# Performance work log

Measured on AMD Instinct MI355X. Metric: run time of the kernel, lower is better.

The kernel has to match this reference:

```python
import jax, jax.numpy as jnp
import numpy as np

N_NODES = 100000
N_HEDGES = 10000
D = 128  # i_d = v_d = e_d = q_d
NUM_CLASS = 10
E = 640000


def _linear_params(key, d_in, d_out):
    k1, k2 = jax.random.split(key)
    lim = 1.0 / np.sqrt(d_in)
    W = jax.random.uniform(k1, (d_in, d_out), jnp.float32, -lim, lim)
    b = jax.random.uniform(k2, (d_out,), jnp.float32, -lim, lim)
    return W, b


def setup_inputs() -> dict:
    key = jax.random.key(0)
    ks = jax.random.split(key, 12)
    vfeat = jax.random.normal(ks[0], (N_NODES, D), jnp.float32)
    efeat = jax.random.normal(ks[1], (N_HEDGES, D), jnp.float32)
    he_idx = jax.random.randint(ks[2], (E,), 0, N_HEDGES, jnp.int32)
    nd_idx = jax.random.randint(ks[3], (E,), 0, N_NODES, jnp.int32)
    Wfl, bfl = _linear_params(ks[4], D, D)   # first_layer_in: i_d -> v_d
    W1, b1 = _linear_params(ks[5], D, D)     # w1: e_d -> q_d
    W2, b2 = _linear_params(ks[6], D, D)     # w2: v_d -> q_d
    W3, b3 = _linear_params(ks[7], D, D)     # w3: v_d -> e_d
    W4, b4 = _linear_params(ks[8], D, D)     # w4: v_d -> q_d
    W5, b5 = _linear_params(ks[9], D, D)     # w5: e_d -> q_d
    W6, b6 = _linear_params(ks[10], D, D)    # w6: e_d -> v_d
    Wc, bc = _linear_params(ks[11], D, NUM_CLASS)
    return dict(vfeat=vfeat, efeat=efeat, he_idx=he_idx, nd_idx=nd_idx,
                first_layer=1, last_layer=1,
                Wfl=Wfl, bfl=bfl, W1=W1, b1=b1, W2=W2, b2=b2, W3=W3, b3=b3,
                W4=W4, b4=b4, W5=W5, b5=b5, W6=W6, b6=b6, Wc=Wc, bc=bc)


def _segment_softmax(logits, segs, num_segments):
    # softmax over the variable-size mailbox of each destination segment
    m = jax.ops.segment_max(logits, segs, num_segments=num_segments)
    m = jnp.where(jnp.isfinite(m), m, 0.0)  # empty segments
    e = jnp.exp(logits - m[segs])
    s = jax.ops.segment_sum(e, segs, num_segments=num_segments)
    return e / jnp.where(s > 0, s, 1.0)[segs]


def reference(vfeat, efeat, he_idx, nd_idx, first_layer, last_layer,
              Wfl, bfl, W1, b1, W2, b2, W3, b3, W4, b4, W5, b5, W6, b6, Wc, bc):
    scale = 1.0 / np.sqrt(D).astype(np.float32)
    # first_layer path (first_layer=1)
    feat_e = efeat @ Wfl + bfl                         # [M, v_d]
    k_e = feat_e @ W5 + b5                             # [M, q_d]
    v_e = feat_e @ W6 + b6                             # [M, v_d]
    q_v = vfeat @ W4 + b4                              # [N, q_d]
    # etype 'con': hyperedge -> node
    attn1 = jax.nn.leaky_relu((k_e[he_idx] * q_v[nd_idx]).sum(-1)) * scale  # [E]
    a1 = _segment_softmax(attn1, nd_idx, N_NODES)
    feat_v = jax.ops.segment_sum(a1[:, None] * v_e[he_idx], nd_idx,
                                 num_segments=N_NODES)  # [N, v_d]
    # etype 'in': node -> hyperedge
    k_v = feat_v @ W2 + b2                             # [N, q_d]
    v_v = feat_v @ W3 + b3                             # [N, e_d]
    q_e = feat_e @ W1 + b1                             # [M, q_d]
    attn2 = jax.nn.leaky_relu((k_v[nd_idx] * q_e[he_idx]).sum(-1)) * scale  # [E]
    a2 = _segment_softmax(attn2, he_idx, N_HEDGES)
    feat_e2 = jax.ops.segment_sum(a2[:, None] * v_v[nd_idx], he_idx,
                                  num_segments=N_HEDGES)  # [M, e_d]
    # last_layer path (last_layer=1): classification head (file save omitted)
    pred = feat_e2 @ Wc + bc                           # [M, num_class]
    return pred
```

## Files before the change

### kernel.cpp

```cpp
#include <hip/hip_runtime.h>
#include <hip/hip_bf16.h>
#include <math.h>


#define HY_M 10000
#define HY_N 100000
#define HY_E 640000

#define SH_N 9
#define NB_N 196
#define SH_M 6
#define NB_M 157

__device__ __forceinline__ unsigned int f2bf(float x) {
    unsigned int u = __float_as_uint(x);
    return (u + 0x7fffu + ((u >> 16) & 1u)) >> 16;
}
__device__ __forceinline__ float2 bf2x2(unsigned int w) {
    float lo = __uint_as_float(w << 16);
    float hi = __uint_as_float(w & 0xffff0000u);
    return make_float2(lo, hi);
}

__global__ void zero_ints(int* __restrict__ p, int n) {
    int i = blockIdx.x * blockDim.x + threadIdx.x;
    if (i < n) p[i] = 0;
}

__global__ void fillk(float* __restrict__ p, float v, int n) {
    int stride = gridDim.x * blockDim.x;
    for (int i = blockIdx.x * blockDim.x + threadIdx.x; i < n; i += stride) p[i] = v;
}

__launch_bounds__(256)
__global__ void coarse_hist(const int* __restrict__ nd, const int* __restrict__ he,
                            int* __restrict__ gcntN, int* __restrict__ gcntM, int E) {
    __shared__ int hN[256], hM[256];
    const int t = threadIdx.x;
    hN[t] = 0; hM[t] = 0;
    __syncthreads();
    const int base = blockIdx.x * 4096;
    for (int i = t; i < 4096; i += 256) {
        int e = base + i;
        if (e < E) {
            atomicAdd(&hN[nd[e] >> SH_N], 1);
            atomicAdd(&hM[he[e] >> SH_M], 1);
        }
    }
    __syncthreads();
    if (hN[t]) atomicAdd(&gcntN[t], hN[t]);
    if (hM[t]) atomicAdd(&gcntM[t], hM[t]);
}

__global__ void coarse_scan(const int* __restrict__ gcntN, const int* __restrict__ gcntM,
                            int* __restrict__ coffN, int* __restrict__ coffM, int E) {
    __shared__ int s[256];
    const int* g = blockIdx.x ? gcntM : gcntN;
    int* o = blockIdx.x ? coffM : coffN;
    const int nb = blockIdx.x ? NB_M : NB_N;
    const int t = threadIdx.x;
    int v = (t < nb) ? g[t] : 0;
    int orig = v;
    s[t] = v; __syncthreads();
    for (int off = 1; off < 256; off <<= 1) {
        int x = (t >= off) ? s[t - off] : 0;
        __syncthreads(); s[t] += x; __syncthreads();
    }
    if (t < nb) o[t] = s[t] - orig;
    if (t == 0) o[nb] = E;
}

__launch_bounds__(256)
__global__ void part_scatter(const int* __restrict__ nd, const int* __restrict__ he,
                             const int* __restrict__ coffN, const int* __restrict__ coffM,
                             int* __restrict__ gcurN, int* __restrict__ gcurM,
                             unsigned int* __restrict__ stN, unsigned int* __restrict__ stM,
                             int E) {
    __shared__ int hN[256], hM[256];
    const int t = threadIdx.x;
    hN[t] = 0; hM[t] = 0;
    __syncthreads();
    const int base = blockIdx.x * 4096;
    for (int i = t; i < 4096; i += 256) {
        int e = base + i;
        if (e < E) {
            atomicAdd(&hN[nd[e] >> SH_N], 1);
            atomicAdd(&hM[he[e] >> SH_M], 1);
        }
    }
    __syncthreads();
    int cN = hN[t], cM = hM[t];
    __syncthreads();
    if (cN) hN[t] = coffN[t] + atomicAdd(&gcurN[t], cN);
    if (cM) hM[t] = coffM[t] + atomicAdd(&gcurM[t], cM);
    __syncthreads();
    for (int i = t; i < 4096; i += 256) {
        int e = base + i;
        if (e < E) {
            int d = nd[e], h = he[e];
            int pN = atomicAdd(&hN[d >> SH_N], 1);
            stN[pN] = ((unsigned int)(d & 511) << 14) | (unsigned int)h;
            int pM = atomicAdd(&hM[h >> SH_M], 1);
            stM[pM] = ((unsigned int)(h & 63) << 17) | (unsigned int)d;
        }
    }
}

__launch_bounds__(256)
__global__ void bucket_build(const unsigned int* __restrict__ stN,
                             const unsigned int* __restrict__ stM,
                             const int* __restrict__ coffN, const int* __restrict__ coffM,
                             int* __restrict__ nd_off, int* __restrict__ he_off,
                             int* __restrict__ nd_adj, int* __restrict__ he_adj) {
    __shared__ int cnt[512];
    __shared__ int cur[512];
    __shared__ int ps[256];
    int b = blockIdx.x;
    const int t = threadIdx.x;
    const unsigned int* st; const int* coff; int* offout; int* adj;
    int dmin, dcnt, sshift; unsigned int smask; int ntot;
    if (b < NB_N) {
        st = stN; coff = coffN; offout = nd_off; adj = nd_adj;
        dmin = b << SH_N; dcnt = min(512, HY_N - dmin);
        sshift = 14; smask = 0x3FFFu; ntot = HY_N;
    } else {
        b -= NB_N;
        st = stM; coff = coffM; offout = he_off; adj = he_adj;
        dmin = b << SH_M; dcnt = min(64, HY_M - dmin);
        sshift = 17; smask = 0x1FFFFu; ntot = HY_M;
    }
    const int cbase = coff[b], cend = coff[b + 1];
    cnt[t] = 0; cnt[t + 256] = 0;
    __syncthreads();
    for (int k = cbase + t; k < cend; k += 256)
        atomicAdd(&cnt[st[k] >> sshift], 1);
    __syncthreads();
    int a0 = cnt[2 * t], a1 = cnt[2 * t + 1];
    int pair = a0 + a1;
    ps[t] = pair;
    __syncthreads();
    for (int off = 1; off < 256; off <<= 1) {
        int x = (t >= off) ? ps[t - off] : 0;
        __syncthreads(); ps[t] += x; __syncthreads();
    }
    int excl = ps[t] - pair;
    cur[2 * t]     = cbase + excl;
    cur[2 * t + 1] = cbase + excl + a0;
    __syncthreads();
    for (int i = t; i < dcnt; i += 256) offout[dmin + i] = cur[i];
    if (t == 0 && dmin + dcnt == ntot) offout[ntot] = cend;
    __syncthreads();
    for (int k = cbase + t; k < cend; k += 256) {
        unsigned int w = st[k];
        int pos = atomicAdd(&cur[w >> sshift], 1);
        adj[pos] = (int)(w & smask);
    }
}

__device__ __forceinline__ void gemm_accum(const float* __restrict__ A,
        const float* __restrict__ W, int nrows, float* wlds,
        float (&acc)[4][4], int row0) {
    const int tid = threadIdx.x;
    const int cg = tid & 31;
    for (int i = tid; i < 4096; i += 512)
        ((float4*)wlds)[i] = ((const float4*)W)[i];
    __syncthreads();
    const float4* A0 = (const float4*)(A + (size_t)min(row0 + 0, nrows - 1) * 128);
    const float4* A1 = (const float4*)(A + (size_t)min(row0 + 1, nrows - 1) * 128);
    const float4* A2 = (const float4*)(A + (size_t)min(row0 + 2, nrows - 1) * 128);
    const float4* A3 = (const float4*)(A + (size_t)min(row0 + 3, nrows - 1) * 128);
    #pragma unroll 2
    for (int kq = 0; kq < 32; ++kq) {
        float4 ar[4] = {A0[kq], A1[kq], A2[kq], A3[kq]};
        const float4* wk = (const float4*)(wlds + kq * 512);
        float4 wr[4] = {wk[cg], wk[32 + cg], wk[64 + cg], wk[96 + cg]};
        #pragma unroll
        for (int r = 0; r < 4; ++r) {
            float av[4] = {ar[r].x, ar[r].y, ar[r].z, ar[r].w};
            #pragma unroll
            for (int j = 0; j < 4; ++j) {
                float wv[4] = {wr[j].x, wr[j].y, wr[j].z, wr[j].w};
                #pragma unroll
                for (int c = 0; c < 4; ++c)
                    acc[r][c] = fmaf(av[j], wv[c], acc[r][c]);
            }
        }
    }
}

__device__ __forceinline__ void gemm_epilogue(const float* __restrict__ b,
        float* __restrict__ Cf, unsigned short* __restrict__ Cb, int ldb, int coloff,
        int nrows, float (&acc)[4][4], int row0) {
    const int cg = threadIdx.x & 31;
    const float4 bv = ((const float4*)b)[cg];
    #pragma unroll
    for (int r = 0; r < 4; ++r) {
        int gr = row0 + r;
        if (gr < nrows) {
            float o0 = acc[r][0] + bv.x, o1 = acc[r][1] + bv.y;
            float o2 = acc[r][2] + bv.z, o3 = acc[r][3] + bv.w;
            if (Cf) {
                float4 o = {o0, o1, o2, o3};
                ((float4*)(Cf + (size_t)gr * 128))[cg] = o;
            }
            if (Cb) {
                uint2 pk;
                pk.x = f2bf(o0) | (f2bf(o1) << 16);
                pk.y = f2bf(o2) | (f2bf(o3) << 16);
                *(uint2*)(Cb + (size_t)gr * ldb + coloff + cg * 4) = pk;
            }
        }
    }
}

__launch_bounds__(512)
__global__ void gemm_uni(const float* __restrict__ A, const float* __restrict__ W,
                         const float* __restrict__ b, float* __restrict__ Cf,
                         unsigned short* __restrict__ Cb, int ldb, int coloff, int nrows) {
    __shared__ __align__(16) float wlds[16384];
    const int rs = threadIdx.x >> 5;
    const int row0 = blockIdx.x * 64 + rs * 4;
    float acc[4][4] = {};
    gemm_accum(A, W, nrows, wlds, acc, row0);
    gemm_epilogue(b, Cf, Cb, ldb, coloff, nrows, acc, row0);
}

__launch_bounds__(512)
__global__ void gemm_pair(const float* __restrict__ Aa, const float* __restrict__ Wa,
                          float* __restrict__ Ca,
                          const float* __restrict__ Ab, const float* __restrict__ Wb,
                          float* __restrict__ Cb2, const float* __restrict__ zb) {
    __shared__ __align__(16) float wlds[16384];
    const int rs = threadIdx.x >> 5;
    const int row0 = blockIdx.x * 64 + rs * 4;
    const float* A = blockIdx.y ? Ab : Aa;
    const float* W = blockIdx.y ? Wb : Wa;
    float* C = blockIdx.y ? Cb2 : Ca;
    float acc[4][4] = {};
    gemm_accum(A, W, 128, wlds, acc, row0);
    gemm_epilogue(zb, C, nullptr, 0, 0, 128, acc, row0);
}

__launch_bounds__(512)
__global__ void gemm_x3(const float* __restrict__ A,
        const float* __restrict__ W54, const float* __restrict__ b54,
        const float* __restrict__ W6, const float* __restrict__ b6,
        const float* __restrict__ W12, const float* __restrict__ b12,
        unsigned short* __restrict__ kv, float* __restrict__ qt, int nrows) {
    __shared__ __align__(16) float wlds[16384];
    const int rs = threadIdx.x >> 5;
    const int row0 = blockIdx.x * 64 + rs * 4;
    const int y = blockIdx.y;
    const float* W = y == 0 ? W54 : (y == 1 ? W6 : W12);
    const float* b = y == 0 ? b54 : (y == 1 ? b6 : b12);
    float acc[4][4] = {};
    gemm_accum(A, W, nrows, wlds, acc, row0);
    if (y == 2) gemm_epilogue(b, qt, nullptr, 0, 0, nrows, acc, row0);
    else        gemm_epilogue(b, nullptr, kv, 256, y == 0 ? 0 : 128, nrows, acc, row0);
}

__global__ void transpose2(const float* __restrict__ W2, const float* __restrict__ W4,
                           float* __restrict__ W2T, float* __restrict__ W4T) {
    int i = blockIdx.x * 256 + threadIdx.x;
    const float* s = blockIdx.y ? W4 : W2;
    float* d = blockIdx.y ? W4T : W2T;
    if (i < 128 * 128) d[(i & 127) * 128 + (i >> 7)] = s[i];
}

__global__ void prep_vecs(const float* __restrict__ WX, const float* __restrict__ WY,
                          const float* __restrict__ bX, const float* __restrict__ bY,
                          float* __restrict__ bXY, float* __restrict__ wXbY,
                          float* __restrict__ sXY) {
    int t = threadIdx.x;
    if (t < 128) {
        float acc = 0.f;
        for (int j = 0; j < 128; ++j) acc += WY[t * 128 + j] * bX[j];
        bXY[t] = acc;
    } else {
        int k = t - 128;
        float acc = 0.f;
        for (int j = 0; j < 128; ++j) acc += WX[k * 128 + j] * bY[j];
        wXbY[k] = acc;
    }
    if (t == 0) {
        float acc = 0.f;
        for (int j = 0; j < 128; ++j) acc += bX[j] * bY[j];
        *sXY = acc;
    }
}

__global__ void prep_w3c(const float* __restrict__ W3, const float* __restrict__ Wc,
                         const float* __restrict__ b3, float* __restrict__ W3c,
                         float* __restrict__ b3c) {
    int i = blockIdx.x * 256 + threadIdx.x;
    if (i < 1280) {
        int k = i / 10, c = i % 10;
        float acc = 0.f;
        for (int j = 0; j < 128; ++j) acc += W3[k * 128 + j] * Wc[j * 10 + c];
        W3c[i] = acc;
    } else if (i < 1290) {
        int c = i - 1280;
        float acc = 0.f;
        for (int j = 0; j < 128; ++j) acc += b3[j] * Wc[j * 10 + c];
        b3c[c] = acc;
    }
}

__launch_bounds__(256)
__global__ void dotc2(const float* __restrict__ X,
                      const float* __restrict__ u1, const float* __restrict__ s1v,
                      const float* __restrict__ u2, const float* __restrict__ s2v,
                      float* __restrict__ o1, float* __restrict__ o2, int M) {
    int w = (blockIdx.x * blockDim.x + threadIdx.x) >> 6;
    int lane = threadIdx.x & 63;
    if (w >= M) return;
    float2 r = ((const float2*)(X + (size_t)w * 128))[lane];
    float2 a1 = ((const float2*)u1)[lane];
    float2 a2 = ((const float2*)u2)[lane];
    float d1 = r.x * a1.x + r.y * a1.y;
    float d2 = r.x * a2.x + r.y * a2.y;
    #pragma unroll
    for (int o = 32; o; o >>= 1) {
        d1 += __shfl_xor(d1, o, 64);
        d2 += __shfl_xor(d2, o, 64);
    }
    if (lane == 0) { o1[w] = d1 + *s1v; o2[w] = d2 + *s2v; }
}

__launch_bounds__(256)
__global__ void attn_s1(const float* __restrict__ vf,
                        const unsigned int* __restrict__ kv,
                        const float* __restrict__ ck,
                        const int* __restrict__ off, const int* __restrict__ adj,
                        unsigned int* __restrict__ fv,
                        int nseg, float scale) {
    int seg = (blockIdx.x * blockDim.x + threadIdx.x) >> 4;
    int j = threadIdx.x & 15;
    if (seg >= nseg) return;
    int beg = off[seg], end = off[seg + 1];
    const float4 qa = ((const float4*)(vf + (size_t)seg * 128 + 8 * j))[0];
    const float4 qb = ((const float4*)(vf + (size_t)seg * 128 + 8 * j))[1];
    float m = -INFINITY, l = 0.f;
    float a[8] = {};
    if (beg < end) {
        int s = adj[beg];
        uint4 kw = ((const uint4*)(kv + (size_t)s * 128))[j];
        uint4 vw = ((const uint4*)(kv + (size_t)s * 128 + 64))[j];
        float ckn = ck[s];
        for (int i = beg; i < end; ++i) {
            uint4 kc = kw, vc = vw;
            float ckc = ckn;
            if (i + 1 < end) {
                int s2 = adj[i + 1];
                kw = ((const uint4*)(kv + (size_t)s2 * 128))[j];
                vw = ((const uint4*)(kv + (size_t)s2 * 128 + 64))[j];
                ckn = ck[s2];
            }
            float2 k0 = bf2x2(kc.x), k1 = bf2x2(kc.y), k2 = bf2x2(kc.z), k3 = bf2x2(kc.w);
            float d = k0.x * qa.x + k0.y * qa.y + k1.x * qa.z + k1.y * qa.w
                    + k2.x * qb.x + k2.y * qb.y + k3.x * qb.z + k3.y * qb.w;
            d += __shfl_xor(d, 8); d += __shfl_xor(d, 4);
            d += __shfl_xor(d, 2); d += __shfl_xor(d, 1);
            d += ckc;
            d = (d >= 0.f ? d : 0.01f * d) * scale;
            float2 v0 = bf2x2(vc.x), v1 = bf2x2(vc.y), v2 = bf2x2(vc.z), v3 = bf2x2(vc.w);
            float vfv[8] = {v0.x, v0.y, v1.x, v1.y, v2.x, v2.y, v3.x, v3.y};
            float mn = fmaxf(m, d);
            float r = __expf(m - mn);
            float p = __expf(d - mn);
            l = l * r + p;
            #pragma unroll
            for (int t = 0; t < 8; ++t) a[t] = a[t] * r + p * vfv[t];
            m = mn;
        }
    }
    float inv = (l > 0.f) ? 1.f / l : 0.f;
    uint4 o;
    o.x = f2bf(a[0] * inv) | (f2bf(a[1] * inv) << 16);
    o.y = f2bf(a[2] * inv) | (f2bf(a[3] * inv) << 16);
    o.z = f2bf(a[4] * inv) | (f2bf(a[5] * inv) << 16);
    o.w = f2bf(a[6] * inv) | (f2bf(a[7] * inv) << 16);
    ((uint4*)(fv + (size_t)seg * 64))[j] = o;
}

__launch_bounds__(256)
__global__ void attn_s2(const float* __restrict__ QT, const float* __restrict__ cvec,
                        const unsigned int* __restrict__ fv,
                        const int* __restrict__ off, const int* __restrict__ adj,
                        float* __restrict__ agg, float* __restrict__ flag, float scale) {
    __shared__ float sm[16], sl[16];
    __shared__ float sacc[16][16][9];
    const int seg = blockIdx.x;
    const int g = threadIdx.x >> 4;
    const int j = threadIdx.x & 15;
    const int beg = off[seg], end = off[seg + 1];
    const float4 qa = ((const float4*)(QT + (size_t)seg * 128 + 8 * j))[0];
    const float4 qb = ((const float4*)(QT + (size_t)seg * 128 + 8 * j))[1];
    const float cadd = cvec[seg];
    float m = -INFINITY, l = 0.f;
    float a[8] = {};
    int i = beg + g;
    if (i < end) {
        int s = adj[i];
        uint4 rw = ((const uint4*)(fv + (size_t)s * 64))[j];
        for (; i < end; i += 16) {
            uint4 rc = rw;
            if (i + 16 < end) {
                int s2 = adj[i + 16];
                rw = ((const uint4*)(fv + (size_t)s2 * 64))[j];
            }
            float2 r0 = bf2x2(rc.x), r1 = bf2x2(rc.y), r2 = bf2x2(rc.z), r3 = bf2x2(rc.w);
            float rf[8] = {r0.x, r0.y, r1.x, r1.y, r2.x, r2.y, r3.x, r3.y};
            float d = rf[0] * qa.x + rf[1] * qa.y + rf[2] * qa.z + rf[3] * qa.w
                    + rf[4] * qb.x + rf[5] * qb.y + rf[6] * qb.z + rf[7] * qb.w;
            d += __shfl_xor(d, 8); d += __shfl_xor(d, 4);
            d += __shfl_xor(d, 2); d += __shfl_xor(d, 1);
            d += cadd;
            d = (d >= 0.f ? d : 0.01f * d) * scale;
            float mn = fmaxf(m, d);
            float r = __expf(m - mn);
            float p = __expf(d - mn);
            l = l * r + p;
            #pragma unroll
            for (int t = 0; t < 8; ++t) a[t] = a[t] * r + p * rf[t];
            m = mn;
        }
    }
    if (j == 0) { sm[g] = m; sl[g] = l; }
    #pragma unroll
    for (int t = 0; t < 8; ++t) sacc[g][j][t] = a[t];
    __syncthreads();
    if (threadIdx.x < 16) {
        float M2 = -INFINITY;
        #pragma unroll 4
        for (int gg = 0; gg < 16; ++gg) if (sl[gg] > 0.f) M2 = fmaxf(M2, sm[gg]);
        float L = 0.f;
        float acc[8] = {};
        #pragma unroll 4
        for (int gg = 0; gg < 16; ++gg) {
            float f = (sl[gg] > 0.f) ? __expf(sm[gg] - M2) : 0.f;
            L += f * sl[gg];
            #pragma unroll
            for (int t = 0; t < 8; ++t) acc[t] += f * sacc[gg][threadIdx.x][t];
        }
        float inv = (L > 0.f) ? 1.f / L : 0.f;
        float4 o1 = {acc[0] * inv, acc[1] * inv, acc[2] * inv, acc[3] * inv};
        float4 o2 = {acc[4] * inv, acc[5] * inv, acc[6] * inv, acc[7] * inv};
        ((float4*)(agg + (size_t)seg * 128 + 8 * threadIdx.x))[0] = o1;
        ((float4*)(agg + (size_t)seg * 128 + 8 * threadIdx.x))[1] = o2;
        if (threadIdx.x == 0) flag[seg] = (L > 0.f) ? 1.f : 0.f;
    }
}

__global__ void head2(const float* __restrict__ agg, const float* __restrict__ flag,
                      const float* __restrict__ W3c, const float* __restrict__ b3c,
                      const float* __restrict__ bc, float* __restrict__ out, int M) {
    int t = blockIdx.x * blockDim.x + threadIdx.x;
    if (t >= M * 10) return;
    int row = t / 10, c = t % 10;
    float acc = bc[c] + flag[row] * b3c[c];
    #pragma unroll 8
    for (int k = 0; k < 128; ++k)
        acc = fmaf(agg[(size_t)row * 128 + k], W3c[k * 10 + c], acc);
    out[t] = acc;
}

extern "C" void kernel_launch(void* const* d_in, const int* in_sizes, int n_in,
                              void* d_out, int out_size, void* d_ws, size_t ws_size,
                              hipStream_t stream) {
    const float* vfeat = (const float*)d_in[0];
    const float* efeat = (const float*)d_in[1];
    const int*   he    = (const int*)d_in[2];
    const int*   nd    = (const int*)d_in[3];
    const float* Wfl = (const float*)d_in[6],  *bfl = (const float*)d_in[7];
    const float* W1  = (const float*)d_in[8],  *b1  = (const float*)d_in[9];
    const float* W2  = (const float*)d_in[10], *b2  = (const float*)d_in[11];
    const float* W3  = (const float*)d_in[12], *b3  = (const float*)d_in[13];
    const float* W4  = (const float*)d_in[14], *b4  = (const float*)d_in[15];
    const float* W5  = (const float*)d_in[16], *b5  = (const float*)d_in[17];
    const float* W6  = (const float*)d_in[18], *b6  = (const float*)d_in[19];
    const float* Wc  = (const float*)d_in[20], *bc  = (const float*)d_in[21];
    float* out = (float*)d_out;
    float* ws  = (float*)d_ws;

    const int M = HY_M, N = HY_N, E = HY_E;

    float* feat_e = ws + 0;
    float* qt_e   = ws + 1280000;
    float* agg    = ws + 2560000;
    float* c_e    = ws + 3840000;
    float* ck     = ws + 3850000;
    float* flag   = ws + 3860000;
    float* W2T    = ws + 3870000;
    float* W4T    = ws + 3886384;
    float* W12    = ws + 3902768;
    float* W54    = ws + 3919152;
    float* W3c    = ws + 3935536;
    float* b3c    = ws + 3936816;
    float* b12    = ws + 3936832;
    float* w1b2   = ws + 3936960;
    float* s12    = ws + 3937088;
    float* b54    = ws + 3937092;
    float* w5b4   = ws + 3937220;
    float* s54    = ws + 3937348;
    float* zeros  = ws + 3937352;
    unsigned int* kv_bf = (unsigned int*)(ws + 3937480);
    unsigned int* fv_bf = kv_bf + (size_t)M * 128;
    int* nd_off = (int*)(fv_bf + (size_t)N * 64);
    int* he_off = nd_off + 100001;
    int* nd_adj = he_off + 10001;
    int* he_adj = nd_adj + 640000;
    unsigned int* stN = (unsigned int*)(he_adj + 640000);
    unsigned int* stM = stN + 640000;
    int* gcntN = (int*)(stM + 640000);
    int* gcntM = gcntN + 256;
    int* gcurN = gcntM + 256;
    int* gcurM = gcurN + 256;
    int* coffN = gcurM + 256;
    int* coffM = coffN + 256;

    const float scale = 0.08838834764831843f;
    const int nchunk = (E + 4095) / 4096;

    zero_ints<<<4, 256, 0, stream>>>(gcntN, 1024);
    coarse_hist<<<nchunk, 256, 0, stream>>>(nd, he, gcntN, gcntM, E);
    coarse_scan<<<2, 256, 0, stream>>>(gcntN, gcntM, coffN, coffM, E);
    part_scatter<<<nchunk, 256, 0, stream>>>(nd, he, coffN, coffM,
                                             gcurN, gcurM, stN, stM, E);
    bucket_build<<<NB_N + NB_M, 256, 0, stream>>>(stN, stM, coffN, coffM,
                                                  nd_off, he_off, nd_adj, he_adj);

    transpose2<<<dim3(64, 2), 256, 0, stream>>>(W2, W4, W2T, W4T);
    fillk<<<1, 128, 0, stream>>>(zeros, 0.f, 128);
    prep_vecs<<<1, 256, 0, stream>>>(W1, W2, b1, b2, b12, w1b2, s12);
    prep_vecs<<<1, 256, 0, stream>>>(W5, W4, b5, b4, b54, w5b4, s54);
    gemm_pair<<<dim3(2, 2), 512, 0, stream>>>(W1, W2T, W12, W5, W4T, W54, zeros);
    prep_w3c<<<6, 256, 0, stream>>>(W3, Wc, b3, W3c, b3c);

    gemm_uni<<<(M + 63) / 64, 512, 0, stream>>>(efeat, Wfl, bfl, feat_e,
                                                nullptr, 0, 0, M);
    gemm_x3<<<dim3((M + 63) / 64, 3), 512, 0, stream>>>(
        feat_e, W54, b54, W6, b6, W12, b12, (unsigned short*)kv_bf, qt_e, M);
    dotc2<<<(M * 64 + 255) / 256, 256, 0, stream>>>(feat_e, w1b2, s12,
                                                    w5b4, s54, c_e, ck, M);

    attn_s1<<<(N * 16 + 255) / 256, 256, 0, stream>>>(
        vfeat, kv_bf, ck, nd_off, nd_adj, fv_bf, N, scale);

    attn_s2<<<M, 256, 0, stream>>>(qt_e, c_e, fv_bf, he_off, he_adj, agg, flag, scale);

    head2<<<(M * 10 + 255) / 256, 256, 0, stream>>>(agg, flag, W3c, b3c, bc, out, M);
}
```

Before: 220.3 us.

## Fold first-layer weights into downstream projections and sort nodes by degree

Precomputes the products Wfl@W54, Wfl@W6 and Wfl@W12 and the matching folded biases, so the per-hyperedge projections read efeat directly. This removes the feat_e GEMM and its intermediate buffer. The M-row GEMM is rewritten as a smaller-tile kernel spread across six blocks in y. Separately, it builds a permutation that orders nodes by degree, so each wavefront in attn_s1 handles segments of similar length and suffers less divergence. In exchange it adds three extra tiny kernels plus more setup launches, the folded weights change rounding slightly, and the permuted order makes vfeat and output accesses less contiguous.

```diff
diff --git a/kernel.cpp b/kernel.cpp
--- a/kernel.cpp
+++ b/kernel.cpp
@@ -118,15 +118,15 @@
     int b = blockIdx.x;
     const int t = threadIdx.x;
     const unsigned int* st; const int* coff; int* offout; int* adj;
-    int dmin, dcnt, sshift; unsigned int smask; int ntot;
+    int dmin, dcnt2, sshift; unsigned int smask; int ntot;
     if (b < NB_N) {
         st = stN; coff = coffN; offout = nd_off; adj = nd_adj;
-        dmin = b << SH_N; dcnt = min(512, HY_N - dmin);
+        dmin = b << SH_N; dcnt2 = min(512, HY_N - dmin);
         sshift = 14; smask = 0x3FFFu; ntot = HY_N;
     } else {
         b -= NB_N;
         st = stM; coff = coffM; offout = he_off; adj = he_adj;
-        dmin = b << SH_M; dcnt = min(64, HY_M - dmin);
+        dmin = b << SH_M; dcnt2 = min(64, HY_M - dmin);
         sshift = 17; smask = 0x1FFFFu; ntot = HY_M;
     }
     const int cbase = coff[b], cend = coff[b + 1];
@@ -147,13 +147,44 @@
     cur[2 * t]     = cbase + excl;
     cur[2 * t + 1] = cbase + excl + a0;
     __syncthreads();
-    for (int i = t; i < dcnt; i += 256) offout[dmin + i] = cur[i];
-    if (t == 0 && dmin + dcnt == ntot) offout[ntot] = cend;
+    for (int i = t; i < dcnt2; i += 256) offout[dmin + i] = cur[i];
+    if (t == 0 && dmin + dcnt2 == ntot) offout[ntot] = cend;
     __syncthreads();
     for (int k = cbase + t; k < cend; k += 256) {
         unsigned int w = st[k];
         int pos = atomicAdd(&cur[w >> sshift], 1);
         adj[pos] = (int)(w & smask);
+    }
+}
+
+__global__ void deg_hist(const int* __restrict__ off, int* __restrict__ dcnt, int n) {
+    __shared__ int h[64];
+    int t = threadIdx.x;
+    if (t < 64) h[t] = 0;
+    __syncthreads();
+    int i = blockIdx.x * blockDim.x + t;
+    if (i < n) atomicAdd(&h[min(off[i + 1] - off[i], 63)], 1);
+    __syncthreads();
+    if (t < 64 && h[t]) atomicAdd(&dcnt[t], h[t]);
+}
+
+__global__ void deg_scan(const int* __restrict__ dcnt, int* __restrict__ dcur) {
+    int t = threadIdx.x;
+    int v = dcnt[t];
+    int s = v;
+    for (int o = 1; o < 64; o <<= 1) {
+        int x = __shfl_up(s, o, 64);
+        if (t >= o) s += x;
+    }
+    dcur[t] = s - v;
+}
+
+__global__ void deg_scatter(const int* __restrict__ off, int* __restrict__ dcur,
+                            int* __restrict__ nperm, int n) {
+    int i = blockIdx.x * blockDim.x + threadIdx.x;
+    if (i < n) {
+        int p = atomicAdd(&dcur[min(off[i + 1] - off[i], 63)], 1);
+        nperm[p] = i;
     }
 }
 
@@ -188,41 +219,19 @@
     }
 }
 
-__device__ __forceinline__ void gemm_epilogue(const float* __restrict__ b,
-        float* __restrict__ Cf, unsigned short* __restrict__ Cb, int ldb, int coloff,
-        int nrows, float (&acc)[4][4], int row0) {
+__device__ __forceinline__ void gemm_store_f32(const float* __restrict__ b,
+        float* __restrict__ Cf, int nrows, float (&acc)[4][4], int row0) {
     const int cg = threadIdx.x & 31;
     const float4 bv = ((const float4*)b)[cg];
     #pragma unroll
     for (int r = 0; r < 4; ++r) {
         int gr = row0 + r;
         if (gr < nrows) {
-            float o0 = acc[r][0] + bv.x, o1 = acc[r][1] + bv.y;
-            float o2 = acc[r][2] + bv.z, o3 = acc[r][3] + bv.w;
-            if (Cf) {
-                float4 o = {o0, o1, o2, o3};
-                ((float4*)(Cf + (size_t)gr * 128))[cg] = o;
-            }
-            if (Cb) {
-                uint2 pk;
-                pk.x = f2bf(o0) | (f2bf(o1) << 16);
-                pk.y = f2bf(o2) | (f2bf(o3) << 16);
-                *(uint2*)(Cb + (size_t)gr * ldb + coloff + cg * 4) = pk;
-            }
-        }
-    }
-}
-
-__launch_bounds__(512)
-__global__ void gemm_uni(const float* __restrict__ A, const float* __restrict__ W,
-                         const float* __restrict__ b, float* __restrict__ Cf,
-                         unsigned short* __restrict__ Cb, int ldb, int coloff, int nrows) {
-    __shared__ __align__(16) float wlds[16384];
-    const int rs = threadIdx.x >> 5;
-    const int row0 = blockIdx.x * 64 + rs * 4;
-    float acc[4][4] = {};
-    gemm_accum(A, W, nrows, wlds, acc, row0);
-    gemm_epilogue(b, Cf, Cb, ldb, coloff, nrows, acc, row0);
+            float4 o = {acc[r][0] + bv.x, acc[r][1] + bv.y,
+                        acc[r][2] + bv.z, acc[r][3] + bv.w};
+            ((float4*)(Cf + (size_t)gr * 128))[cg] = o;
+        }
+    }
 }
 
 __launch_bounds__(512)
@@ -238,25 +247,81 @@
     float* C = blockIdx.y ? Cb2 : Ca;
     float acc[4][4] = {};
     gemm_accum(A, W, 128, wlds, acc, row0);
-    gemm_epilogue(zb, C, nullptr, 0, 0, 128, acc, row0);
+    gemm_store_f32(zb, C, 128, acc, row0);
 }
 
 __launch_bounds__(512)
-__global__ void gemm_x3(const float* __restrict__ A,
-        const float* __restrict__ W54, const float* __restrict__ b54,
-        const float* __restrict__ W6, const float* __restrict__ b6,
-        const float* __restrict__ W12, const float* __restrict__ b12,
-        unsigned short* __restrict__ kv, float* __restrict__ qt, int nrows) {
+__global__ void gemm_trip(const float* __restrict__ Wfl,
+        const float* __restrict__ W54, const float* __restrict__ W6,
+        const float* __restrict__ W12, float* __restrict__ Wk,
+        float* __restrict__ Wv, float* __restrict__ Wq, const float* __restrict__ zb) {
     __shared__ __align__(16) float wlds[16384];
     const int rs = threadIdx.x >> 5;
     const int row0 = blockIdx.x * 64 + rs * 4;
-    const int y = blockIdx.y;
-    const float* W = y == 0 ? W54 : (y == 1 ? W6 : W12);
-    const float* b = y == 0 ? b54 : (y == 1 ? b6 : b12);
+    const float* W = blockIdx.y == 0 ? W54 : (blockIdx.y == 1 ? W6 : W12);
+    float* C = blockIdx.y == 0 ? Wk : (blockIdx.y == 1 ? Wv : Wq);
     float acc[4][4] = {};
-    gemm_accum(A, W, nrows, wlds, acc, row0);
-    if (y == 2) gemm_epilogue(b, qt, nullptr, 0, 0, nrows, acc, row0);
-    else        gemm_epilogue(b, nullptr, kv, 256, y == 0 ? 0 : 128, nrows, acc, row0);
+    gemm_accum(Wfl, W, 128, wlds, acc, row0);
+    gemm_store_f32(zb, C, 128, acc, row0);
+}
+
+__launch_bounds__(256)
+__global__ void gemm_m(const float* __restrict__ A,
+        const float* __restrict__ Wk, const float* __restrict__ bk,
+        const float* __restrict__ Wv, const float* __restrict__ bvv,
+        const float* __restrict__ Wq, const float* __restrict__ bq,
+        unsigned short* __restrict__ kv, float* __restrict__ qt, int nrows) {
+    __shared__ __align__(16) float wlds[128 * 64];
+    const int tid = threadIdx.x;
+    const int mat = blockIdx.y >> 1;
+    const int half = blockIdx.y & 1;
+    const float* W = mat == 0 ? Wk : (mat == 1 ? Wv : Wq);
+    const float* bb = mat == 0 ? bk : (mat == 1 ? bvv : bq);
+    const float4* W4 = (const float4*)W;
+    float4* wl4 = (float4*)wlds;
+    for (int i = tid; i < 2048; i += 256)
+        wl4[i] = W4[(i >> 4) * 32 + half * 16 + (i & 15)];
+    __syncthreads();
+    const int cg = tid & 15;
+    const int rs = tid >> 4;
+    const int row0 = blockIdx.x * 32 + rs * 2;
+    const float4* A0 = (const float4*)(A + (size_t)min(row0, nrows - 1) * 128);
+    const float4* A1 = (const float4*)(A + (size_t)min(row0 + 1, nrows - 1) * 128);
+    float acc[2][4] = {};
+    #pragma unroll 4
+    for (int kq = 0; kq < 32; ++kq) {
+        float4 a0 = A0[kq], a1 = A1[kq];
+        float av0[4] = {a0.x, a0.y, a0.z, a0.w};
+        float av1[4] = {a1.x, a1.y, a1.z, a1.w};
+        #pragma unroll
+        for (int jj = 0; jj < 4; ++jj) {
+            float4 w4 = wl4[(4 * kq + jj) * 16 + cg];
+            float wv4[4] = {w4.x, w4.y, w4.z, w4.w};
+            #pragma unroll
+            for (int c = 0; c < 4; ++c) {
+                acc[0][c] = fmaf(av0[jj], wv4[c], acc[0][c]);
+                acc[1][c] = fmaf(av1[jj], wv4[c], acc[1][c]);
+            }
+        }
+    }
+    const float4 bv4 = ((const float4*)bb)[half * 16 + cg];
+    #pragma unroll
+    for (int r = 0; r < 2; ++r) {
+        int gr = row0 + r;
+        if (gr < nrows) {
+            float o0 = acc[r][0] + bv4.x, o1 = acc[r][1] + bv4.y;
+            float o2 = acc[r][2] + bv4.z, o3 = acc[r][3] + bv4.w;
+            if (mat == 2) {
+                float4 o = {o0, o1, o2, o3};
+                ((float4*)(qt + (size_t)gr * 128))[half * 16 + cg] = o;
+            } else {
+                uint2 pk;
+                pk.x = f2bf(o0) | (f2bf(o1) << 16);
+                pk.y = f2bf(o2) | (f2bf(o3) << 16);
+                *(uint2*)(kv + (size_t)gr * 256 + mat * 128 + half * 64 + cg * 4) = pk;
+            }
+        }
+    }
 }
 
 __global__ void transpose2(const float* __restrict__ W2, const float* __restrict__ W4,
@@ -289,6 +354,47 @@
     }
 }
 
+__global__ void prep_fold(const float* __restrict__ Wfl, const float* __restrict__ bfl,
+                          const float* __restrict__ W54, const float* __restrict__ b54v,
+                          const float* __restrict__ W6, const float* __restrict__ b6,
+                          const float* __restrict__ W12, const float* __restrict__ b12v,
+                          const float* __restrict__ w1b2, const float* __restrict__ s12,
+                          const float* __restrict__ w5b4, const float* __restrict__ s54,
+                          float* __restrict__ bk, float* __restrict__ bv,
+                          float* __restrict__ bq, float* __restrict__ u_c,
+                          float* __restrict__ u_k, float* __restrict__ t_c,
+                          float* __restrict__ t_k) {
+    int t = threadIdx.x;
+    if (t < 128) {
+        float a1 = 0.f, a2 = 0.f, a3 = 0.f;
+        for (int j = 0; j < 128; ++j) {
+            float f = bfl[j];
+            a1 += f * W54[j * 128 + t];
+            a2 += f * W6[j * 128 + t];
+            a3 += f * W12[j * 128 + t];
+        }
+        bk[t] = a1 + b54v[t];
+        bv[t] = a2 + b6[t];
+        bq[t] = a3 + b12v[t];
+    } else {
+        int k = t - 128;
+        float a1 = 0.f, a2 = 0.f;
+        for (int j = 0; j < 128; ++j) {
+            float f = Wfl[k * 128 + j];
+            a1 += f * w1b2[j];
+            a2 += f * w5b4[j];
+        }
+        u_c[k] = a1;
+        u_k[k] = a2;
+    }
+    if (t == 0) {
+        float a1 = 0.f, a2 = 0.f;
+        for (int j = 0; j < 128; ++j) { a1 += bfl[j] * w1b2[j]; a2 += bfl[j] * w5b4[j]; }
+        *t_c = a1 + *s12;
+        *t_k = a2 + *s54;
+    }
+}
+
 __global__ void prep_w3c(const float* __restrict__ W3, const float* __restrict__ Wc,
                          const float* __restrict__ b3, float* __restrict__ W3c,
                          float* __restrict__ b3c) {
@@ -308,8 +414,8 @@
 
 __launch_bounds__(256)
 __global__ void dotc2(const float* __restrict__ X,
-                      const float* __restrict__ u1, const float* __restrict__ s1v,
-                      const float* __restrict__ u2, const float* __restrict__ s2v,
+                      const float* __restrict__ u1, const float* __restrict__ t1v,
+                      const float* __restrict__ u2, const float* __restrict__ t2v,
                       float* __restrict__ o1, float* __restrict__ o2, int M) {
     int w = (blockIdx.x * blockDim.x + threadIdx.x) >> 6;
     int lane = threadIdx.x & 63;
@@ -324,7 +430,7 @@
         d1 += __shfl_xor(d1, o, 64);
         d2 += __shfl_xor(d2, o, 64);
     }
-    if (lane == 0) { o1[w] = d1 + *s1v; o2[w] = d2 + *s2v; }
+    if (lane == 0) { o1[w] = d1 + *t1v; o2[w] = d2 + *t2v; }
 }
 
 __launch_bounds__(256)
@@ -332,11 +438,13 @@
                         const unsigned int* __restrict__ kv,
                         const float* __restrict__ ck,
                         const int* __restrict__ off, const int* __restrict__ adj,
+                        const int* __restrict__ nperm,
                         unsigned int* __restrict__ fv,
                         int nseg, float scale) {
-    int seg = (blockIdx.x * blockDim.x + threadIdx.x) >> 4;
+    int slot = (blockIdx.x * blockDim.x + threadIdx.x) >> 4;
     int j = threadIdx.x & 15;
-    if (seg >= nseg) return;
+    if (slot >= nseg) return;
+    int seg = nperm[slot];
     int beg = off[seg], end = off[seg + 1];
     const float4 qa = ((const float4*)(vf + (size_t)seg * 128 + 8 * j))[0];
     const float4 qb = ((const float4*)(vf + (size_t)seg * 128 + 8 * j))[1];
@@ -485,44 +593,56 @@
 
     const int M = HY_M, N = HY_N, E = HY_E;
 
-    float* feat_e = ws + 0;
-    float* qt_e   = ws + 1280000;
-    float* agg    = ws + 2560000;
-    float* c_e    = ws + 3840000;
-    float* ck     = ws + 3850000;
-    float* flag   = ws + 3860000;
-    float* W2T    = ws + 3870000;
-    float* W4T    = ws + 3886384;
-    float* W12    = ws + 3902768;
-    float* W54    = ws + 3919152;
-    float* W3c    = ws + 3935536;
-    float* b3c    = ws + 3936816;
-    float* b12    = ws + 3936832;
-    float* w1b2   = ws + 3936960;
-    float* s12    = ws + 3937088;
-    float* b54    = ws + 3937092;
-    float* w5b4   = ws + 3937220;
-    float* s54    = ws + 3937348;
-    float* zeros  = ws + 3937352;
-    unsigned int* kv_bf = (unsigned int*)(ws + 3937480);
+    float* qt_e  = ws + 0;
+    float* agg   = ws + 1280000;
+    float* c_e   = ws + 2560000;
+    float* ck    = ws + 2570000;
+    float* flag  = ws + 2580000;
+    float* W2T   = ws + 2590000;
+    float* W4T   = ws + 2606384;
+    float* W12   = ws + 2622768;
+    float* W54   = ws + 2639152;
+    float* Wk    = ws + 2655536;
+    float* Wv    = ws + 2671920;
+    float* Wq    = ws + 2688304;
+    float* W3c   = ws + 2704688;
+    float* b3c   = ws + 2705968;
+    float* b12v  = ws + 2705984;
+    float* w1b2  = ws + 2706112;
+    float* s12   = ws + 2706240;
+    float* b54v  = ws + 2706244;
+    float* w5b4  = ws + 2706372;
+    float* s54   = ws + 2706500;
+    float* bk    = ws + 2706504;
+    float* bv    = ws + 2706632;
+    float* bq    = ws + 2706760;
+    float* u_c   = ws + 2706888;
+    float* u_k   = ws + 2707016;
+    float* t_c   = ws + 2707144;
+    float* t_k   = ws + 2707148;
+    float* zeros = ws + 2707152;
+    unsigned int* kv_bf = (unsigned int*)(ws + 2707280);
     unsigned int* fv_bf = kv_bf + (size_t)M * 128;
     int* nd_off = (int*)(fv_bf + (size_t)N * 64);
     int* he_off = nd_off + 100001;
     int* nd_adj = he_off + 10001;
     int* he_adj = nd_adj + 640000;
-    unsigned int* stN = (unsigned int*)(he_adj + 640000);
+    int* nperm  = he_adj + 640000;
+    unsigned int* stN = (unsigned int*)(nperm + 100000);
     unsigned int* stM = stN + 640000;
     int* gcntN = (int*)(stM + 640000);
     int* gcntM = gcntN + 256;
     int* gcurN = gcntM + 256;
     int* gcurM = gcurN + 256;
-    int* coffN = gcurM + 256;
+    int* dcnt  = gcurM + 256;
+    int* dcur  = dcnt + 64;
+    int* coffN = dcur + 64;
     int* coffM = coffN + 256;
 
     const float scale = 0.08838834764831843f;
     const int nchunk = (E + 4095) / 4096;
 
-    zero_ints<<<4, 256, 0, stream>>>(gcntN, 1024);
+    zero_ints<<<5, 256, 0, stream>>>(gcntN, 1152);
     coarse_hist<<<nchunk, 256, 0, stream>>>(nd, he, gcntN, gcntM, E);
     coarse_scan<<<2, 256, 0, stream>>>(gcntN, gcntM, coffN, coffM, E);
     part_scatter<<<nchunk, 256, 0, stream>>>(nd, he, coffN, coffM,
@@ -530,22 +650,28 @@
     bucket_build<<<NB_N + NB_M, 256, 0, stream>>>(stN, stM, coffN, coffM,
                                                   nd_off, he_off, nd_adj, he_adj);
 
+    deg_hist<<<(N + 255) / 256, 256, 0, stream>>>(nd_off, dcnt, N);
+    deg_scan<<<1, 64, 0, stream>>>(dcnt, dcur);
+    deg_scatter<<<(N + 255) / 256, 256, 0, stream>>>(nd_off, dcur, nperm, N);
+
     transpose2<<<dim3(64, 2), 256, 0, stream>>>(W2, W4, W2T, W4T);
     fillk<<<1, 128, 0, stream>>>(zeros, 0.f, 128);
-    prep_vecs<<<1, 256, 0, stream>>>(W1, W2, b1, b2, b12, w1b2, s12);
-    prep_vecs<<<1, 256, 0, stream>>>(W5, W4, b5, b4, b54, w5b4, s54);
+    prep_vecs<<<1, 256, 0, stream>>>(W1, W2, b1, b2, b12v, w1b2, s12);
+    prep_vecs<<<1, 256, 0, stream>>>(W5, W4, b5, b4, b54v, w5b4, s54);
     gemm_pair<<<dim3(2, 2), 512, 0, stream>>>(W1, W2T, W12, W5, W4T, W54, zeros);
+    gemm_trip<<<dim3(2, 3), 512, 0, stream>>>(Wfl, W54, W6, W12, Wk, Wv, Wq, zeros);
+    prep_fold<<<1, 256, 0, stream>>>(Wfl, bfl, W54, b54v, W6, b6, W12, b12v,
+                                     w1b2, s12, w5b4, s54,
+                                     bk, bv, bq, u_c, u_k, t_c, t_k);
     prep_w3c<<<6, 256, 0, stream>>>(W3, Wc, b3, W3c, b3c);
 
-    gemm_uni<<<(M + 63) / 64, 512, 0, stream>>>(efeat, Wfl, bfl, feat_e,
-                                                nullptr, 0, 0, M);
-    gemm_x3<<<dim3((M + 63) / 64, 3), 512, 0, stream>>>(
-        feat_e, W54, b54, W6, b6, W12, b12, (unsigned short*)kv_bf, qt_e, M);
-    dotc2<<<(M * 64 + 255) / 256, 256, 0, stream>>>(feat_e, w1b2, s12,
-                                                    w5b4, s54, c_e, ck, M);
+    gemm_m<<<dim3((M + 31) / 32, 6), 256, 0, stream>>>(
+        efeat, Wk, bk, Wv, bv, Wq, bq, (unsigned short*)kv_bf, qt_e, M);
+    dotc2<<<(M * 64 + 255) / 256, 256, 0, stream>>>(efeat, u_c, t_c, u_k, t_k,
+                                                    c_e, ck, M);
 
     attn_s1<<<(N * 16 + 255) / 256, 256, 0, stream>>>(
-        vfeat, kv_bf, ck, nd_off, nd_adj, fv_bf, N, scale);
+        vfeat, kv_bf, ck, nd_off, nd_adj, nperm, fv_bf, N, scale);
 
     attn_s2<<<M, 256, 0, stream>>>(qt_e, c_e, fv_bf, he_off, he_adj, agg, flag, scale);
 
```

After: 598.4 us. +171.6%, slower.
